# Performance work log

Measured on AMD Instinct MI355X. Metric: run time of the kernel, lower is better.

Reference implementation:

```python
import jax, jax.numpy as jnp
import numpy as np
import math

INPUT_DIM = 1024
EMBED_DIM = 1024
NUM_HEADS = 16
HEAD_DIM = EMBED_DIM // NUM_HEADS


def setup_inputs() -> dict:
    key = jax.random.key(0)
    k_x, k_qkv, k_out_w, k_out_b = jax.random.split(key, 4)
    x = jax.random.normal(k_x, (1, 4096, INPUT_DIM), dtype=jnp.float32)
    # nn.Linear weights are [out, in]; kaiming-uniform-ish scale
    s1 = 1.0 / math.sqrt(INPUT_DIM)
    s2 = 1.0 / math.sqrt(EMBED_DIM)
    qkv_w = jax.random.uniform(k_qkv, (3 * EMBED_DIM, INPUT_DIM), jnp.float32, -s1, s1)
    out_w = jax.random.uniform(k_out_w, (EMBED_DIM, EMBED_DIM), jnp.float32, -s2, s2)
    out_b = jax.random.uniform(k_out_b, (EMBED_DIM,), jnp.float32, -s2, s2)
    return {"x": x, "qkv_w": qkv_w, "out_w": out_w, "out_b": out_b}


def reference(x, qkv_w, out_w, out_b):
    B, N, C = x.shape
    qkv = jnp.einsum('bnc,ec->bne', x, qkv_w)  # [B,N,3E]
    q = qkv[:, :, 0:EMBED_DIM].reshape(B, N, NUM_HEADS, HEAD_DIM)
    k = qkv[:, :, EMBED_DIM:2 * EMBED_DIM].reshape(B, N, NUM_HEADS, HEAD_DIM)
    v = qkv[:, :, 2 * EMBED_DIM:].reshape(B, N, NUM_HEADS, HEAD_DIM)
    scores = jnp.einsum('bihd,bjhd->bhij', q, k) / jnp.sqrt(jnp.float32(HEAD_DIM))
    attn = jax.nn.softmax(scores, axis=-1)  # [B,H,N,N]
    out = jnp.einsum('bhik,bkhd->bhid', attn, v)
    out = out.transpose(0, 2, 1, 3).reshape(B, N, EMBED_DIM)
    return jnp.einsum('bne,fe->bnf', out, out_w) + out_b
```

## Files before the change

### kernel.cpp

```cpp
#include <hip/hip_runtime.h>
#include <hip/hip_bf16.h>

typedef __bf16 bf16;
typedef bf16 bf16x8 __attribute__((ext_vector_type(8)));
typedef bf16 bf16x4 __attribute__((ext_vector_type(4)));
typedef float f32x4 __attribute__((ext_vector_type(4)));

#define MFMA16(a, b, c) __builtin_amdgcn_mfma_f32_16x16x32_bf16(a, b, c, 0, 0, 0)

__device__ __forceinline__ void g2l16(const bf16* g, bf16* l) {
  __builtin_amdgcn_global_load_lds(
      (__attribute__((address_space(1))) void*)(void*)g,
      (__attribute__((address_space(3))) void*)l,
      16, 0, 0);
}

__device__ __forceinline__ int sniff_inblock(const void* x, int tid) {
  __shared__ int sf;
  if (tid < 64) {
    unsigned short v = ((const unsigned short*)x)[tid];
    int e = (v >> 7) & 0xFF;
    int sane = (e == 0) || (e >= 112 && e <= 142);
    unsigned long long m = __ballot(sane);
    if (tid == 0) sf = (__popcll(m) >= 56) ? 1 : 0;
  }
  __syncthreads();
  return sf;
}

__device__ __forceinline__ void conv8(const void* in, bf16* out, long i, int f) {
  if (f) {
    ((bf16x8*)out)[i] = ((const bf16x8*)in)[i];
  } else {
    const float4* p = (const float4*)in;
    float4 a = p[i * 2], b = p[i * 2 + 1];
    bf16x8 v;
    v[0] = (bf16)a.x; v[1] = (bf16)a.y; v[2] = (bf16)a.z; v[3] = (bf16)a.w;
    v[4] = (bf16)b.x; v[5] = (bf16)b.y; v[6] = (bf16)b.z; v[7] = (bf16)b.w;
    ((bf16x8*)out)[i] = v;
  }
}

__global__ void convert2_to_bf16(const void* __restrict__ a, bf16* __restrict__ oa,
                                 long na8, const void* __restrict__ b,
                                 bf16* __restrict__ ob, long nb8,
                                 const void* __restrict__ x) {
  const int f = sniff_inblock(x, threadIdx.x);
  long i = (long)blockIdx.x * 256 + threadIdx.x;
  if (i < na8) conv8(a, oa, i, f);
  else if (i - na8 < nb8) conv8(b, ob, i - na8, f);
}

__global__ __launch_bounds__(256) void gemm_qkv(
    const bf16* __restrict__ A, const bf16* __restrict__ B,
    bf16* __restrict__ qB, bf16* __restrict__ kP, bf16* __restrict__ vP) {
  __shared__ __align__(16) bf16 As[128 * 32];
  __shared__ __align__(16) bf16 Bs[128 * 32];

  const int tid  = threadIdx.x;
  const int lane = tid & 63;
  const int wave = tid >> 6;
  const int wm   = wave >> 1, wn = wave & 1;
  const int l15  = lane & 15, quad = lane >> 4;
  const long m0 = (long)blockIdx.x * 128;
  const long n0 = (long)blockIdx.y * 128;
  const int  K  = 1024;

  const bf16* Ab = A + m0 * K;
  const bf16* Bb = B + n0 * K;
  const int rowA = tid & 127;
  const int dc   = tid >> 7;

  f32x4 acc[4][4] = {};

  for (int k0 = 0; k0 < K; k0 += 32) {
    g2l16(Ab + (long)rowA * K + k0 + dc * 8,       As + tid * 8);
    g2l16(Ab + (long)rowA * K + k0 + (dc + 2) * 8, As + (tid + 256) * 8);
    g2l16(Bb + (long)rowA * K + k0 + dc * 8,       Bs + tid * 8);
    g2l16(Bb + (long)rowA * K + k0 + (dc + 2) * 8, Bs + (tid + 256) * 8);
    __syncthreads();

    bf16x8 af[4], bfr[4];
#pragma unroll
    for (int t = 0; t < 4; t++) {
      af[t]  = *(const bf16x8*)(As + (quad * 128 + wm * 64 + t * 16 + l15) * 8);
      bfr[t] = *(const bf16x8*)(Bs + (quad * 128 + wn * 64 + t * 16 + l15) * 8);
    }
#pragma unroll
    for (int tm = 0; tm < 4; tm++)
#pragma unroll
      for (int tn = 0; tn < 4; tn++)
        acc[tm][tn] = MFMA16(af[tm], bfr[tn], acc[tm][tn]);
    __syncthreads();
  }

  const long rb = m0 + wm * 64;
  const long cb = n0 + wn * 64;
  const int third = (int)(n0 >> 10);
  const float QSC = 0.125f * 1.44269504088896f;

#pragma unroll
  for (int tm = 0; tm < 4; tm++) {
#pragma unroll
    for (int tn = 0; tn < 4; tn++) {
      const long r0 = rb + tm * 16 + quad * 4;
      const long c  = cb + tn * 16 + l15;
      if (third == 0) {
#pragma unroll
        for (int r = 0; r < 4; r++)
          qB[(r0 + r) * 1024 + c] = (bf16)(acc[tm][tn][r] * QSC);
      } else if (third == 1) {
        const int ep = (int)c - 1024;
        const int h = ep >> 6, d = ep & 63;
        const int n0r = (int)r0;
        const int kt = n0r >> 6;
        const int kh = (n0r >> 5) & 1;
        const int t_ = (n0r >> 2) & 1;
        const int mq = (n0r >> 3) & 3;
        const long base = ((long)h * 64 + kt) * 4096 +
                          (((d >> 3) * 64) + kh * 32 + t_ * 16 + mq * 4) * 8 +
                          (d & 7);
#pragma unroll
        for (int r = 0; r < 4; r++)
          kP[base + r * 8] = (bf16)acc[tm][tn][r];
      } else {
        const int ep = (int)c - 2048;
        const int h = ep >> 6, d = ep & 63;
        const int n0r = (int)r0;
        const int kt = n0r >> 6;
        const int kh = (n0r >> 5) & 1;
        const int kq = (n0r >> 3) & 3;
        bf16x4 v;
#pragma unroll
        for (int r = 0; r < 4; r++) v[r] = (bf16)acc[tm][tn][r];
        *(bf16x4*)(vP + ((long)h * 64 + kt) * 4096 +
                   (kh * 256 + kq * 64 + d) * 8 + (quad & 1) * 4) = v;
      }
    }
  }
}

template <bool BIAS, bool DYNOUT>
__global__ __launch_bounds__(256) void gemm_bt(
    const bf16* __restrict__ A, const bf16* __restrict__ B,
    void* __restrict__ Cv, const bf16* __restrict__ bias,
    int M, int Nn, int K, const void* __restrict__ xs) {
  __shared__ __align__(16) bf16 As[128 * 32];
  __shared__ __align__(16) bf16 Bs[128 * 32];

  const int tid  = threadIdx.x;
  const int obf = DYNOUT ? sniff_inblock(xs, tid) : 1;

  const int lane = tid & 63;
  const int wave = tid >> 6;
  const int wm   = wave >> 1, wn = wave & 1;
  const int l15  = lane & 15, quad = lane >> 4;
  const long m0 = (long)blockIdx.x * 128;
  const long n0 = (long)blockIdx.y * 128;

  const bf16* Ab = A + m0 * K;
  const bf16* Bb = B + n0 * K;
  const int rowA = tid & 127;
  const int dc   = tid >> 7;

  f32x4 acc[4][4] = {};

  for (int k0 = 0; k0 < K; k0 += 32) {
    g2l16(Ab + (long)rowA * K + k0 + dc * 8,       As + tid * 8);
    g2l16(Ab + (long)rowA * K + k0 + (dc + 2) * 8, As + (tid + 256) * 8);
    g2l16(Bb + (long)rowA * K + k0 + dc * 8,       Bs + tid * 8);
    g2l16(Bb + (long)rowA * K + k0 + (dc + 2) * 8, Bs + (tid + 256) * 8);
    __syncthreads();

    bf16x8 af[4], bfr[4];
#pragma unroll
    for (int t = 0; t < 4; t++) {
      af[t]  = *(const bf16x8*)(As + (quad * 128 + wm * 64 + t * 16 + l15) * 8);
      bfr[t] = *(const bf16x8*)(Bs + (quad * 128 + wn * 64 + t * 16 + l15) * 8);
    }
#pragma unroll
    for (int tm = 0; tm < 4; tm++)
#pragma unroll
      for (int tn = 0; tn < 4; tn++)
        acc[tm][tn] = MFMA16(af[tm], bfr[tn], acc[tm][tn]);
    __syncthreads();
  }

  const long rb = m0 + wm * 64;
  const long cb = n0 + wn * 64;
#pragma unroll
  for (int tm = 0; tm < 4; tm++) {
#pragma unroll
    for (int tn = 0; tn < 4; tn++) {
      const long r0 = rb + tm * 16 + quad * 4;
      const long c  = cb + tn * 16 + l15;
      const float bv = BIAS ? (float)bias[c] : 0.0f;
#pragma unroll
      for (int r = 0; r < 4; r++) {
        const float val = acc[tm][tn][r] + bv;
        const long idx = (r0 + r) * Nn + c;
        if (DYNOUT && !obf) ((float*)Cv)[idx] = val;
        else                ((bf16*)Cv)[idx]  = (bf16)val;
      }
    }
  }
}

__device__ __forceinline__ void attn_tile(
    int kt, const bf16* kb, const bf16* vb, int quad, int koff, int voff,
    const bf16x8 (&qf)[4][2], const bf16x8 (&kcur)[2][2], bf16x8 (&knxt)[2][2],
    const bf16x8& onesf, f32x4 (&oa)[4][4], f32x4 (&la)[4]) {
  bf16x8 vf[4];
  const bf16* vt = vb + (long)kt * 4096;
#pragma unroll
  for (int dt = 0; dt < 4; dt++)
    vf[dt] = *(const bf16x8*)(vt + dt * 128 + voff);

  f32x4 s[4][2];
#pragma unroll
  for (int t = 0; t < 2; t++) {
    __builtin_amdgcn_s_setprio(1);
#pragma unroll
    for (int g = 0; g < 4; g++) {
      f32x4 z = {};
      z = MFMA16(kcur[t][0], qf[g][0], z);
      z = MFMA16(kcur[t][1], qf[g][1], z);
      s[g][t] = z;
    }
    __builtin_amdgcn_s_setprio(0);
  }

  const bf16* kn = kb + (long)(kt + 1) * 4096;
#pragma unroll
  for (int t = 0; t < 2; t++)
#pragma unroll
    for (int j = 0; j < 2; j++)
      knxt[t][j] = *(const bf16x8*)(kn + (j * 4 + quad) * 512 + t * 128 + koff);

  bf16x8 pf[4];
#pragma unroll
  for (int g = 0; g < 4; g++) {
    union { bf16x8 v; __hip_bfloat162 h2[4]; } u;
#pragma unroll
    for (int idx = 0; idx < 4; idx++) {
      const int t = idx >> 1, rr = (idx & 1) * 2;
      float p0 = __builtin_amdgcn_exp2f(s[g][t][rr]);
      float p1 = __builtin_amdgcn_exp2f(s[g][t][rr + 1]);
      u.h2[idx] = __float22bfloat162_rn(float2{p0, p1});
    }
    pf[g] = u.v;
  }

#pragma unroll
  for (int dt = 0; dt < 4; dt++) {
    __builtin_amdgcn_s_setprio(1);
#pragma unroll
    for (int g = 0; g < 4; g++) oa[g][dt] = MFMA16(vf[dt], pf[g], oa[g][dt]);
    __builtin_amdgcn_s_setprio(0);
  }
  __builtin_amdgcn_s_setprio(1);
#pragma unroll
  for (int g = 0; g < 4; g++) la[g] = MFMA16(onesf, pf[g], la[g]);
  __builtin_amdgcn_s_setprio(0);
}

__global__ __launch_bounds__(128, 2) void flash_attn(
    const bf16* __restrict__ qB, const bf16* __restrict__ kP,
    const bf16* __restrict__ vP, bf16* __restrict__ O) {
  __shared__ __align__(16) float red[4096];
  __shared__ float lred[256];

  const int tid = threadIdx.x;
  const int lane = tid & 63;
  const int kh = tid >> 6;
  const int l15 = lane & 15, quad = lane >> 4;
  const int bid = blockIdx.x;
  const int xcd = bid & 7, bi = bid >> 3;
  const int h  = xcd + 8 * (bi >> 6);
  const int qt = bi & 63;
  const int q0 = qt * 64;

  {
    const int slot = (bid >> 8) & 3;
    if (slot == 1)      __builtin_amdgcn_s_sleep(10);
    else if (slot == 2) __builtin_amdgcn_s_sleep(20);
    else if (slot == 3) __builtin_amdgcn_s_sleep(30);
  }

  bf16x8 qf[4][2];
#pragma unroll
  for (int g = 0; g < 4; g++) {
    const bf16* qrow = qB + (long)(q0 + g * 16 + l15) * 1024 + h * 64;
    qf[g][0] = *(const bf16x8*)(qrow + quad * 8);
    qf[g][1] = *(const bf16x8*)(qrow + 32 + quad * 8);
  }

  bf16x8 onesf;
#pragma unroll
  for (int j = 0; j < 8; j++) onesf[j] = (bf16)1.0f;

  f32x4 oa[4][4] = {};
  f32x4 la[4] = {};

  const bf16* kb = kP + (long)h * 64 * 4096;
  const bf16* vb = vP + (long)h * 64 * 4096;

  const int koff = (kh * 32 + l15) * 8;
  const int voff = (kh * 256 + quad * 64 + l15) * 8;

  bf16x8 kA[2][2], kB[2][2];
#pragma unroll
  for (int t = 0; t < 2; t++)
#pragma unroll
    for (int j = 0; j < 2; j++)
      kA[t][j] = *(const bf16x8*)(kb + (j * 4 + quad) * 512 + t * 128 + koff);

#pragma unroll 1
  for (int kt = 0; kt < 64; kt += 2) {
    attn_tile(kt,     kb, vb, quad, koff, voff, qf, kA, kB, onesf, oa, la);
    attn_tile(kt + 1, kb, vb, quad, koff, voff, qf, kB, kA, onesf, oa, la);
  }

  if (kh == 1) {
#pragma unroll
    for (int g = 0; g < 4; g++)
#pragma unroll
      for (int dt = 0; dt < 4; dt++)
        *(f32x4*)(red + (g * 4 + dt) * 256 + lane * 4) = oa[g][dt];
#pragma unroll
    for (int g = 0; g < 4; g++) lred[g * 64 + lane] = la[g][0];
  }
  __syncthreads();
  if (kh == 0) {
#pragma unroll
    for (int g = 0; g < 4; g++) {
#pragma unroll
      for (int dt = 0; dt < 4; dt++)
        oa[g][dt] += *(const f32x4*)(red + (g * 4 + dt) * 256 + lane * 4);
      const float l = la[g][0] + lred[g * 64 + lane];
      const float inv = 1.0f / l;
      bf16* orow = O + (long)(q0 + g * 16 + l15) * 1024 + h * 64;
#pragma unroll
      for (int dt = 0; dt < 4; dt++) {
        bf16x4 v;
#pragma unroll
        for (int r = 0; r < 4; r++) v[r] = (bf16)(oa[g][dt][r] * inv);
        *(bf16x4*)(orow + dt * 16 + quad * 4) = v;
      }
    }
  }
}

extern "C" void kernel_launch(void* const* d_in, const int* in_sizes, int n_in,
                              void* d_out, int out_size, void* d_ws, size_t ws_size,
                              hipStream_t stream) {
  const void* x     = d_in[0];
  const void* qkv_w = d_in[1];
  const void* out_w = d_in[2];
  const void* out_b = d_in[3];

  char* ws = (char*)d_ws;
  bf16* qB   = (bf16*)(ws);
  bf16* kP   = (bf16*)(ws + 8388608);
  bf16* vP   = (bf16*)(ws + 16777216);
  bf16* ob   = (bf16*)(ws + 25165824);
  bf16* qwb  = (bf16*)(ws + 33554432);
  bf16* xb   = ob;
  bf16* owb  = qB;
  bf16* obb  = qB + 1048576;

  convert2_to_bf16<<<3584, 256, 0, stream>>>(x, xb, 524288, qkv_w, qwb, 393216, x);

  gemm_qkv<<<dim3(32, 24), 256, 0, stream>>>(xb, qwb, qB, kP, vP);

  flash_attn<<<1024, 128, 0, stream>>>(qB, kP, vP, ob);

  convert2_to_bf16<<<513, 256, 0, stream>>>(out_w, owb, 131072, out_b, obb, 128, x);

  gemm_bt<true, true><<<dim3(32, 8), 256, 0, stream>>>(
      ob, owb, d_out, obb, 4096, 1024, 1024, x);
}
```

Before: 233.2 us.

## Skew attention loop so QK of next tile overlaps exp and PV of previous

Restructures the flash-attention inner loop into a software pipeline. Each iteration computes the QK scores for tile i while the exp2/bf16 packing and PV accumulation use the scores and V fragments of tile i-1. A prologue and an epilogue handle the first and last tiles. The aim is to hide transcendental/VALU latency behind MFMA work, at the cost of extra live registers (the carried score array and a second V fragment buffer), which could cause spills under the existing launch bounds.

```diff
diff --git a/kernel.cpp b/kernel.cpp
--- a/kernel.cpp
+++ b/kernel.cpp
@@ -206,38 +206,7 @@
   }
 }
 
-__device__ __forceinline__ void attn_tile(
-    int kt, const bf16* kb, const bf16* vb, int quad, int koff, int voff,
-    const bf16x8 (&qf)[4][2], const bf16x8 (&kcur)[2][2], bf16x8 (&knxt)[2][2],
-    const bf16x8& onesf, f32x4 (&oa)[4][4], f32x4 (&la)[4]) {
-  bf16x8 vf[4];
-  const bf16* vt = vb + (long)kt * 4096;
-#pragma unroll
-  for (int dt = 0; dt < 4; dt++)
-    vf[dt] = *(const bf16x8*)(vt + dt * 128 + voff);
-
-  f32x4 s[4][2];
-#pragma unroll
-  for (int t = 0; t < 2; t++) {
-    __builtin_amdgcn_s_setprio(1);
-#pragma unroll
-    for (int g = 0; g < 4; g++) {
-      f32x4 z = {};
-      z = MFMA16(kcur[t][0], qf[g][0], z);
-      z = MFMA16(kcur[t][1], qf[g][1], z);
-      s[g][t] = z;
-    }
-    __builtin_amdgcn_s_setprio(0);
-  }
-
-  const bf16* kn = kb + (long)(kt + 1) * 4096;
-#pragma unroll
-  for (int t = 0; t < 2; t++)
-#pragma unroll
-    for (int j = 0; j < 2; j++)
-      knxt[t][j] = *(const bf16x8*)(kn + (j * 4 + quad) * 512 + t * 128 + koff);
-
-  bf16x8 pf[4];
+__device__ __forceinline__ void exp2pack(const f32x4 (&s)[4][2], bf16x8 (&pf)[4]) {
 #pragma unroll
   for (int g = 0; g < 4; g++) {
     union { bf16x8 v; __hip_bfloat162 h2[4]; } u;
@@ -250,7 +219,11 @@
     }
     pf[g] = u.v;
   }
-
+}
+
+__device__ __forceinline__ void pv_accum(
+    const bf16x8 (&vf)[4], const bf16x8 (&pf)[4], const bf16x8& onesf,
+    f32x4 (&oa)[4][4], f32x4 (&la)[4]) {
 #pragma unroll
   for (int dt = 0; dt < 4; dt++) {
     __builtin_amdgcn_s_setprio(1);
@@ -262,6 +235,44 @@
 #pragma unroll
   for (int g = 0; g < 4; g++) la[g] = MFMA16(onesf, pf[g], la[g]);
   __builtin_amdgcn_s_setprio(0);
+}
+
+__device__ __forceinline__ void skew_tile(
+    int i, const bf16* kb, const bf16* vb, int quad, int koff, int voff,
+    const bf16x8 (&qf)[4][2],
+    const bf16x8 (&kcur)[2][2], bf16x8 (&knxt)[2][2],
+    const bf16x8 (&vprev)[4], bf16x8 (&vcur)[4],
+    f32x4 (&sP)[4][2], const bf16x8& onesf,
+    f32x4 (&oa)[4][4], f32x4 (&la)[4]) {
+  const bf16* vt = vb + (long)i * 4096;
+#pragma unroll
+  for (int dt = 0; dt < 4; dt++)
+    vcur[dt] = *(const bf16x8*)(vt + dt * 128 + voff);
+
+  bf16x8 pf[4];
+  exp2pack(sP, pf);
+
+#pragma unroll
+  for (int t = 0; t < 2; t++) {
+    __builtin_amdgcn_s_setprio(1);
+#pragma unroll
+    for (int g = 0; g < 4; g++) {
+      f32x4 z = {};
+      z = MFMA16(kcur[t][0], qf[g][0], z);
+      z = MFMA16(kcur[t][1], qf[g][1], z);
+      sP[g][t] = z;
+    }
+    __builtin_amdgcn_s_setprio(0);
+  }
+
+  const bf16* kn = kb + (long)(i + 1) * 4096;
+#pragma unroll
+  for (int t = 0; t < 2; t++)
+#pragma unroll
+    for (int j = 0; j < 2; j++)
+      knxt[t][j] = *(const bf16x8*)(kn + (j * 4 + quad) * 512 + t * 128 + koff);
+
+  pv_accum(vprev, pf, onesf, oa, la);
 }
 
 __global__ __launch_bounds__(128, 2) void flash_attn(
@@ -301,6 +312,7 @@
 
   f32x4 oa[4][4] = {};
   f32x4 la[4] = {};
+  f32x4 sP[4][2];
 
   const bf16* kb = kP + (long)h * 64 * 4096;
   const bf16* vb = vP + (long)h * 64 * 4096;
@@ -309,16 +321,46 @@
   const int voff = (kh * 256 + quad * 64 + l15) * 8;
 
   bf16x8 kA[2][2], kB[2][2];
+  bf16x8 vfA[4], vfB[4];
+
 #pragma unroll
   for (int t = 0; t < 2; t++)
 #pragma unroll
     for (int j = 0; j < 2; j++)
       kA[t][j] = *(const bf16x8*)(kb + (j * 4 + quad) * 512 + t * 128 + koff);
+#pragma unroll
+  for (int dt = 0; dt < 4; dt++)
+    vfA[dt] = *(const bf16x8*)(vb + dt * 128 + voff);
+
+#pragma unroll
+  for (int t = 0; t < 2; t++) {
+    __builtin_amdgcn_s_setprio(1);
+#pragma unroll
+    for (int g = 0; g < 4; g++) {
+      f32x4 z = {};
+      z = MFMA16(kA[t][0], qf[g][0], z);
+      z = MFMA16(kA[t][1], qf[g][1], z);
+      sP[g][t] = z;
+    }
+    __builtin_amdgcn_s_setprio(0);
+  }
+#pragma unroll
+  for (int t = 0; t < 2; t++)
+#pragma unroll
+    for (int j = 0; j < 2; j++)
+      kB[t][j] = *(const bf16x8*)(kb + 4096 + (j * 4 + quad) * 512 + t * 128 + koff);
 
 #pragma unroll 1
-  for (int kt = 0; kt < 64; kt += 2) {
-    attn_tile(kt,     kb, vb, quad, koff, voff, qf, kA, kB, onesf, oa, la);
-    attn_tile(kt + 1, kb, vb, quad, koff, voff, qf, kB, kA, onesf, oa, la);
+  for (int i = 1; i < 63; i += 2) {
+    skew_tile(i,     kb, vb, quad, koff, voff, qf, kB, kA, vfA, vfB, sP, onesf, oa, la);
+    skew_tile(i + 1, kb, vb, quad, koff, voff, qf, kA, kB, vfB, vfA, sP, onesf, oa, la);
+  }
+  skew_tile(63, kb, vb, quad, koff, voff, qf, kB, kA, vfA, vfB, sP, onesf, oa, la);
+
+  {
+    bf16x8 pf[4];
+    exp2pack(sP, pf);
+    pv_accum(vfB, pf, onesf, oa, la);
   }
 
   if (kh == 1) {
```

Measured after the change: 235.3 us. No clear change (+0.9%).

## Split KV tiles across two wave pairs per block with tree reduction

Applied to the files above, without the earlier changes.

Doubles the flash attention block to 256 threads so that two wave pairs split the key tiles by parity: each pair handles alternate tiles and prefetches the tile two steps ahead. Partial outputs and row sums are combined in shared memory by a two-stage reduction using a doubled reduction buffer. This halves the serial KV loop per wave and raises the number of waves per block, meant to hide latency better. In exchange it costs more shared memory, extra barriers and reduction work, and the prefetch on the final iterations reads past the last tile.

```diff
diff --git a/kernel.cpp b/kernel.cpp
--- a/kernel.cpp
+++ b/kernel.cpp
@@ -230,7 +230,7 @@
     __builtin_amdgcn_s_setprio(0);
   }
 
-  const bf16* kn = kb + (long)(kt + 1) * 4096;
+  const bf16* kn = kb + (long)(kt + 2) * 4096;
 #pragma unroll
   for (int t = 0; t < 2; t++)
 #pragma unroll
@@ -264,15 +264,17 @@
   __builtin_amdgcn_s_setprio(0);
 }
 
-__global__ __launch_bounds__(128, 2) void flash_attn(
+__global__ __launch_bounds__(256, 4) void flash_attn(
     const bf16* __restrict__ qB, const bf16* __restrict__ kP,
     const bf16* __restrict__ vP, bf16* __restrict__ O) {
-  __shared__ __align__(16) float red[4096];
-  __shared__ float lred[256];
+  __shared__ __align__(16) float red[2][4096];
+  __shared__ float lred[2][256];
 
   const int tid = threadIdx.x;
   const int lane = tid & 63;
-  const int kh = tid >> 6;
+  const int wave = tid >> 6;
+  const int kh  = wave & 1;
+  const int par = wave >> 1;
   const int l15 = lane & 15, quad = lane >> 4;
   const int bid = blockIdx.x;
   const int xcd = bid & 7, bi = bid >> 3;
@@ -309,35 +311,62 @@
   const int voff = (kh * 256 + quad * 64 + l15) * 8;
 
   bf16x8 kA[2][2], kB[2][2];
-#pragma unroll
-  for (int t = 0; t < 2; t++)
-#pragma unroll
-    for (int j = 0; j < 2; j++)
-      kA[t][j] = *(const bf16x8*)(kb + (j * 4 + quad) * 512 + t * 128 + koff);
+  {
+    const bf16* k0p = kb + (long)par * 4096;
+#pragma unroll
+    for (int t = 0; t < 2; t++)
+#pragma unroll
+      for (int j = 0; j < 2; j++)
+        kA[t][j] = *(const bf16x8*)(k0p + (j * 4 + quad) * 512 + t * 128 + koff);
+  }
 
 #pragma unroll 1
-  for (int kt = 0; kt < 64; kt += 2) {
-    attn_tile(kt,     kb, vb, quad, koff, voff, qf, kA, kB, onesf, oa, la);
-    attn_tile(kt + 1, kb, vb, quad, koff, voff, qf, kB, kA, onesf, oa, la);
-  }
-
-  if (kh == 1) {
+  for (int j = 0; j < 32; j += 2) {
+    attn_tile(par + 2 * j,       kb, vb, quad, koff, voff, qf, kA, kB, onesf, oa, la);
+    attn_tile(par + 2 * (j + 1), kb, vb, quad, koff, voff, qf, kB, kA, onesf, oa, la);
+  }
+
+  float lv[4];
+#pragma unroll
+  for (int g = 0; g < 4; g++) lv[g] = la[g][0];
+
+  if (par == 1) {
 #pragma unroll
     for (int g = 0; g < 4; g++)
 #pragma unroll
       for (int dt = 0; dt < 4; dt++)
-        *(f32x4*)(red + (g * 4 + dt) * 256 + lane * 4) = oa[g][dt];
-#pragma unroll
-    for (int g = 0; g < 4; g++) lred[g * 64 + lane] = la[g][0];
+        *(f32x4*)(red[kh] + (g * 4 + dt) * 256 + lane * 4) = oa[g][dt];
+#pragma unroll
+    for (int g = 0; g < 4; g++) lred[kh][g * 64 + lane] = lv[g];
   }
   __syncthreads();
-  if (kh == 0) {
+  if (par == 0) {
 #pragma unroll
     for (int g = 0; g < 4; g++) {
 #pragma unroll
       for (int dt = 0; dt < 4; dt++)
-        oa[g][dt] += *(const f32x4*)(red + (g * 4 + dt) * 256 + lane * 4);
-      const float l = la[g][0] + lred[g * 64 + lane];
+        oa[g][dt] += *(const f32x4*)(red[kh] + (g * 4 + dt) * 256 + lane * 4);
+      lv[g] += lred[kh][g * 64 + lane];
+    }
+  }
+  __syncthreads();
+  if (par == 0 && kh == 1) {
+#pragma unroll
+    for (int g = 0; g < 4; g++)
+#pragma unroll
+      for (int dt = 0; dt < 4; dt++)
+        *(f32x4*)(red[0] + (g * 4 + dt) * 256 + lane * 4) = oa[g][dt];
+#pragma unroll
+    for (int g = 0; g < 4; g++) lred[0][g * 64 + lane] = lv[g];
+  }
+  __syncthreads();
+  if (par == 0 && kh == 0) {
+#pragma unroll
+    for (int g = 0; g < 4; g++) {
+#pragma unroll
+      for (int dt = 0; dt < 4; dt++)
+        oa[g][dt] += *(const f32x4*)(red[0] + (g * 4 + dt) * 256 + lane * 4);
+      const float l = lv[g] + lred[0][g * 64 + lane];
       const float inv = 1.0f / l;
       bf16* orow = O + (long)(q0 + g * 16 + l15) * 1024 + h * 64;
 #pragma unroll
@@ -373,7 +402,7 @@
 
   gemm_qkv<<<dim3(32, 24), 256, 0, stream>>>(xb, qwb, qB, kP, vP);
 
-  flash_attn<<<1024, 128, 0, stream>>>(qB, kP, vP, ob);
+  flash_attn<<<1024, 256, 0, stream>>>(qB, kP, vP, ob);
 
   convert2_to_bf16<<<513, 256, 0, stream>>>(out_w, owb, 131072, out_b, obb, 128, x);
 
```

Result: slower. 853.1 us (+265.8%).
